# Kernel tuning notes

Hardware: AMD Instinct MI355X
Metric: run time of the kernel (lower is better)

The kernel has to match this reference:

```python
import jax, jax.numpy as jnp
import numpy as np

N_WORDS, L_CHARS = 16384, 16
CHAR_SIZE, C_EMB = 128, 64
CONV_L, KERNEL, PAD = 256, 3, 2
VOCAB, D_EMB = 50000, 300
PAD_IDX = 1


def setup_inputs() -> dict:
    key = jax.random.key(0)
    k1, k2, k3, k4, k5, k6 = jax.random.split(key, 6)
    X = jax.random.randint(k1, (N_WORDS, L_CHARS), 0, CHAR_SIZE, dtype=jnp.int32)
    X_word = jax.random.randint(k2, (N_WORDS,), 0, VOCAB, dtype=jnp.int32)
    char_emb_w = jax.random.normal(k3, (CHAR_SIZE, C_EMB), dtype=jnp.float32)
    char_emb_w = char_emb_w.at[PAD_IDX].set(0.0)  # padding row zeroed, as in _init_char_embedding
    conv_w = jax.random.normal(k4, (CONV_L, C_EMB, KERNEL), dtype=jnp.float32) * 0.05
    conv_b = jax.random.normal(k5, (CONV_L,), dtype=jnp.float32) * 0.05
    word_emb_w = jax.random.normal(k6, (VOCAB, D_EMB), dtype=jnp.float32)
    return {"X": X, "X_word": X_word, "char_emb_w": char_emb_w,
            "conv_w": conv_w, "conv_b": conv_b, "word_emb_w": word_emb_w}


def reference(X, X_word, char_emb_w, conv_w, conv_b, word_emb_w):
    # char embedding lookup: [N, L, c_emb] -> NCH layout [N, c_emb, L]
    ce = char_emb_w[X].transpose(0, 2, 1)
    # Conv1d(c_emb -> conv_l, kernel=3, padding=2): out length L + 2*PAD - K + 1
    y = jax.lax.conv_general_dilated(
        ce, conv_w, window_strides=(1,), padding=[(PAD, PAD)],
        dimension_numbers=("NCH", "OIH", "NCH"))
    y = jax.nn.relu(y + conv_b[None, :, None])
    # MaxPool over the full time dimension -> [N, conv_l]
    char_feat = jnp.max(y, axis=2)
    # word embedding lookup: [N, d_emb]
    we = word_emb_w[X_word]
    return jnp.concatenate([char_feat, we], axis=1)
```

## Files before the change

kernel.cpp:

```cpp
#include <hip/hip_runtime.h>

#define N_WORDS   16384
#define L_CHARS   16
#define CHAR_SIZE 128
#define C_EMB     64
#define CONV_L    256
#define KERNEL_K  3
#define D_EMB     300
#define OUT_STRIDE (CONV_L + D_EMB)
#define CH_Q      64
#define SLICE_H   (CHAR_SIZE * KERNEL_K * CH_Q)

typedef _Float16 half8 __attribute__((ext_vector_type(8)));

static __device__ __forceinline__ half8 h8max(half8 a, half8 b) {
#if __has_builtin(__builtin_elementwise_max)
    return __builtin_elementwise_max(a, b);
#else
    half8 r;
    #pragma unroll
    for (int i = 0; i < 8; ++i) r[i] = a[i] > b[i] ? a[i] : b[i];
    return r;
#endif
}

__global__ __launch_bounds__(384)
void build_table_fused(const float* __restrict__ emb,
                       const float* __restrict__ w,
                       _Float16* __restrict__ Th) {
    __shared__ float es[CHAR_SIZE * 65];
    __shared__ float ws[C_EMB * KERNEL_K];
    const int o = blockIdx.x;

    for (int idx = threadIdx.x; idx < CHAR_SIZE * C_EMB; idx += 384) {
        int c = idx >> 6, i = idx & 63;
        es[c * 65 + i] = emb[idx];
    }
    if (threadIdx.x < C_EMB * KERNEL_K)
        ws[threadIdx.x] = w[o * (C_EMB * KERNEL_K) + threadIdx.x];
    __syncthreads();

    const int k = threadIdx.x >> 7;
    const int c = threadIdx.x & 127;
    float s = 0.f;
    #pragma unroll
    for (int i = 0; i < C_EMB; ++i)
        s += es[c * 65 + i] * ws[i * KERNEL_K + k];

    Th[(o >> 6) * SLICE_H + c * (KERNEL_K * CH_Q) + k * CH_Q + (o & 63)]
        = (_Float16)s;
}

__global__ __launch_bounds__(256, 3)
void main_kernel(const int* __restrict__ X,
                 const int* __restrict__ Xw,
                 const _Float16* __restrict__ Th,
                 const float* __restrict__ conv_b,
                 const float* __restrict__ word_emb,
                 float* __restrict__ out,
                 int word_blocks) {
    __shared__ __align__(16) _Float16 Ts[SLICE_H];

    const int lane = threadIdx.x & 63;
    const int wv   = threadIdx.x >> 6;

    if ((int)blockIdx.x < word_blocks) {
        const int wavesTotal = word_blocks * 4;
        const int waveId = blockIdx.x * 4 + wv;
        for (int n = waveId; n < N_WORDS; n += 2 * wavesTotal) {
            const int n2 = n + wavesTotal;
            int w0 = Xw[n];
            int w1 = Xw[n2];
            const float4* s0 = (const float4*)(word_emb + (size_t)w0 * D_EMB);
            const float4* s1 = (const float4*)(word_emb + (size_t)w1 * D_EMB);
            const bool tail = lane < (D_EMB / 4 - 64);
            float4 a0 = s0[lane], a1 = s1[lane];
            float4 b0 = {}, b1 = {};
            if (tail) { b0 = s0[64 + lane]; b1 = s1[64 + lane]; }
            float4* d0 = (float4*)(out + (size_t)n  * OUT_STRIDE + CONV_L);
            float4* d1 = (float4*)(out + (size_t)n2 * OUT_STRIDE + CONV_L);
            d0[lane] = a0;
            if (tail) d0[64 + lane] = b0;
            d1[lane] = a1;
            if (tail) d1[64 + lane] = b1;
        }
        return;
    }

    const int cb   = (int)blockIdx.x - word_blocks;
    const int q    = cb & 3;
    const int wgrp = cb >> 2;

    {
        const float4* src = (const float4*)(Th + q * SLICE_H);
        float4* dst = (float4*)Ts;
        #pragma unroll
        for (int i = 0; i < 12; ++i)
            dst[threadIdx.x + i * 256] = src[threadIdx.x + i * 256];
    }
    __syncthreads();

    const int g  = lane >> 3;
    const int l8 = lane & 7;

    float bias[8];
    {
        const float4* bp = (const float4*)(conv_b + q * CH_Q + l8 * 8);
        float4 b0 = bp[0], b1 = bp[1];
        bias[0]=b0.x; bias[1]=b0.y; bias[2]=b0.z; bias[3]=b0.w;
        bias[4]=b1.x; bias[5]=b1.y; bias[6]=b1.z; bias[7]=b1.w;
    }

    int4 c0, c1, c2, c3;
    {
        const int n0 = wgrp * 128 + wv * 8 + g;
        const int4* xr = (const int4*)(X + n0 * L_CHARS);
        c0 = xr[0]; c1 = xr[1]; c2 = xr[2]; c3 = xr[3];
    }

    #pragma unroll
    for (int pass = 0; pass < 4; ++pass) {
        int4 p0 = c0, p1 = c1, p2 = c2, p3 = c3;
        if (pass < 3) {
            const int n1 = wgrp * 128 + (pass + 1) * 32 + wv * 8 + g;
            const int4* xr = (const int4*)(X + n1 * L_CHARS);
            p0 = xr[0]; p1 = xr[1]; p2 = xr[2]; p3 = xr[3];
        }

        const int n = wgrp * 128 + pass * 32 + wv * 8 + g;
        int cs[16] = {c0.x, c0.y, c0.z, c0.w,
                      c1.x, c1.y, c1.z, c1.w,
                      c2.x, c2.y, c2.z, c2.w,
                      c3.x, c3.y, c3.z, c3.w};

        half8 a0 = (half8)(_Float16)0.f;
        half8 a1 = (half8)(_Float16)0.f;
        half8 m  = (half8)(_Float16)(-65504.f);

        #pragma unroll
        for (int j = 0; j < L_CHARS; ++j) {
            const _Float16* row = Ts + cs[j] * (KERNEL_K * CH_Q) + l8 * 8;
            half8 t0 = *(const half8*)(row);
            half8 t1 = *(const half8*)(row + CH_Q);
            half8 t2 = *(const half8*)(row + 2*CH_Q);
            half8 yj = a0 + t2;
            m  = h8max(m, yj);
            a0 = a1 + t1;
            a1 = t0;
        }
        m = h8max(m, a0);
        m = h8max(m, a1);

        float r[8];
        #pragma unroll
        for (int e = 0; e < 8; ++e)
            r[e] = fmaxf((float)m[e] + bias[e], 0.f);
        float4* dst = (float4*)(out + (size_t)n * OUT_STRIDE + q * CH_Q + l8 * 8);
        dst[0] = make_float4(r[0], r[1], r[2], r[3]);
        dst[1] = make_float4(r[4], r[5], r[6], r[7]);

        c0 = p0; c1 = p1; c2 = p2; c3 = p3;
    }
}

extern "C" void kernel_launch(void* const* d_in, const int* in_sizes, int n_in,
                              void* d_out, int out_size, void* d_ws, size_t ws_size,
                              hipStream_t stream) {
    const int*   X    = (const int*)d_in[0];
    const int*   Xw   = (const int*)d_in[1];
    const float* emb  = (const float*)d_in[2];
    const float* w    = (const float*)d_in[3];
    const float* b    = (const float*)d_in[4];
    const float* we   = (const float*)d_in[5];
    float* out = (float*)d_out;

    _Float16* Th = (_Float16*)d_ws;

    build_table_fused<<<CONV_L, 384, 0, stream>>>(emb, w, Th);

    const int WB = 256;
    const int CB = 512;
    main_kernel<<<WB + CB, 256, 0, stream>>>(X, Xw, Th, b, we, out, WB);
}
```

Measured before the change: 123.5 us.

## Fuse char-conv table build into main kernel using split-fp16 MFMA

Removes the separate table-building kernel and its workspace round trip. Each conv block now computes its 128x192 slice of the char-embedding-times-conv-weight table in LDS with fp16 MFMA. Inputs are split into hi/lo halves to keep near-fp32 accuracy, and the LDS layout is XOR-swizzled to avoid bank conflicts. This saves a kernel launch and a global write/read, but every one of the 512 conv blocks recomputes the table slice it needs (each slice is rebuilt by 128 blocks), using strided uncoalesced weight loads.

```diff
diff --git a/kernel.cpp b/kernel.cpp
--- a/kernel.cpp
+++ b/kernel.cpp
@@ -10,8 +10,11 @@
 #define OUT_STRIDE (CONV_L + D_EMB)
 #define CH_Q      64
 #define SLICE_H   (CHAR_SIZE * KERNEL_K * CH_Q)
+#define WROW      (C_EMB * KERNEL_K)
 
 typedef _Float16 half8 __attribute__((ext_vector_type(8)));
+typedef _Float16 half4 __attribute__((ext_vector_type(4)));
+typedef float    f32x4 __attribute__((ext_vector_type(4)));
 
 static __device__ __forceinline__ half8 h8max(half8 a, half8 b) {
 #if __has_builtin(__builtin_elementwise_max)
@@ -24,37 +27,11 @@
 #endif
 }
 
-__global__ __launch_bounds__(384)
-void build_table_fused(const float* __restrict__ emb,
-                       const float* __restrict__ w,
-                       _Float16* __restrict__ Th) {
-    __shared__ float es[CHAR_SIZE * 65];
-    __shared__ float ws[C_EMB * KERNEL_K];
-    const int o = blockIdx.x;
-
-    for (int idx = threadIdx.x; idx < CHAR_SIZE * C_EMB; idx += 384) {
-        int c = idx >> 6, i = idx & 63;
-        es[c * 65 + i] = emb[idx];
-    }
-    if (threadIdx.x < C_EMB * KERNEL_K)
-        ws[threadIdx.x] = w[o * (C_EMB * KERNEL_K) + threadIdx.x];
-    __syncthreads();
-
-    const int k = threadIdx.x >> 7;
-    const int c = threadIdx.x & 127;
-    float s = 0.f;
-    #pragma unroll
-    for (int i = 0; i < C_EMB; ++i)
-        s += es[c * 65 + i] * ws[i * KERNEL_K + k];
-
-    Th[(o >> 6) * SLICE_H + c * (KERNEL_K * CH_Q) + k * CH_Q + (o & 63)]
-        = (_Float16)s;
-}
-
 __global__ __launch_bounds__(256, 3)
 void main_kernel(const int* __restrict__ X,
                  const int* __restrict__ Xw,
-                 const _Float16* __restrict__ Th,
+                 const float* __restrict__ emb,
+                 const float* __restrict__ w,
                  const float* __restrict__ conv_b,
                  const float* __restrict__ word_emb,
                  float* __restrict__ out,
@@ -92,11 +69,77 @@
     const int wgrp = cb >> 2;
 
     {
-        const float4* src = (const float4*)(Th + q * SLICE_H);
-        float4* dst = (float4*)Ts;
+        const int l15 = lane & 15;
+        const int lg  = lane >> 4;
+        const float* wq = w + (size_t)(q * CH_Q) * WROW;
+
         #pragma unroll
-        for (int i = 0; i < 12; ++i)
-            dst[threadIdx.x + i * 256] = src[threadIdx.x + i * 256];
+        for (int ch = 0; ch < 2; ++ch) {
+            f32x4 acc[3][4];
+            #pragma unroll
+            for (int a = 0; a < 3; ++a)
+                #pragma unroll
+                for (int b = 0; b < 4; ++b) acc[a][b] = (f32x4)0.f;
+
+            #pragma unroll
+            for (int kc = 0; kc < 2; ++kc) {
+                half8 Bh[4], Bl[4];
+                #pragma unroll
+                for (int ctl = 0; ctl < 4; ++ctl) {
+                    const int c = (ch * 4 + ctl) * 16 + l15;
+                    const float* ep = emb + c * C_EMB + kc * 32 + lg * 8;
+                    float4 v0 = *(const float4*)ep;
+                    float4 v1 = *(const float4*)(ep + 4);
+                    float vv[8] = {v0.x, v0.y, v0.z, v0.w,
+                                   v1.x, v1.y, v1.z, v1.w};
+                    #pragma unroll
+                    for (int e = 0; e < 8; ++e) {
+                        _Float16 hi = (_Float16)vv[e];
+                        Bh[ctl][e] = hi;
+                        Bl[ctl][e] = (_Float16)(vv[e] - (float)hi);
+                    }
+                }
+                #pragma unroll
+                for (int mt = 0; mt < 3; ++mt) {
+                    const int kk   = (wv * 3 + mt) * 16 + l15;
+                    const int oi   = kk & 63;
+                    const int kpos = kk >> 6;
+                    const float* ap = wq + oi * WROW + kpos
+                                      + (kc * 32 + lg * 8) * KERNEL_K;
+                    half8 Ah, Al;
+                    #pragma unroll
+                    for (int e = 0; e < 8; ++e) {
+                        float v = ap[e * KERNEL_K];
+                        _Float16 hi = (_Float16)v;
+                        Ah[e] = hi;
+                        Al[e] = (_Float16)(v - (float)hi);
+                    }
+                    #pragma unroll
+                    for (int ctl = 0; ctl < 4; ++ctl) {
+                        acc[mt][ctl] = __builtin_amdgcn_mfma_f32_16x16x32_f16(
+                            Ah, Bh[ctl], acc[mt][ctl], 0, 0, 0);
+                        acc[mt][ctl] = __builtin_amdgcn_mfma_f32_16x16x32_f16(
+                            Ah, Bl[ctl], acc[mt][ctl], 0, 0, 0);
+                        acc[mt][ctl] = __builtin_amdgcn_mfma_f32_16x16x32_f16(
+                            Al, Bh[ctl], acc[mt][ctl], 0, 0, 0);
+                    }
+                }
+            }
+            #pragma unroll
+            for (int mt = 0; mt < 3; ++mt) {
+                #pragma unroll
+                for (int ctl = 0; ctl < 4; ++ctl) {
+                    const int kk0 = (wv * 3 + mt) * 16 + lg * 4;
+                    const int c   = (ch * 4 + ctl) * 16 + l15;
+                    half4 pk;
+                    #pragma unroll
+                    for (int r = 0; r < 4; ++r)
+                        pk[r] = (_Float16)acc[mt][ctl][r];
+                    const int byte = c * 384 + ((kk0 * 2) ^ ((c & 7) << 4));
+                    *(half4*)((char*)Ts + byte) = pk;
+                }
+            }
+        }
     }
     __syncthreads();
 
@@ -139,10 +182,11 @@
 
         #pragma unroll
         for (int j = 0; j < L_CHARS; ++j) {
-            const _Float16* row = Ts + cs[j] * (KERNEL_K * CH_Q) + l8 * 8;
+            const int cc = cs[j];
+            const _Float16* row = Ts + cc * 192 + ((l8 ^ (cc & 7)) << 3);
             half8 t0 = *(const half8*)(row);
-            half8 t1 = *(const half8*)(row + CH_Q);
-            half8 t2 = *(const half8*)(row + 2*CH_Q);
+            half8 t1 = *(const half8*)(row + 64);
+            half8 t2 = *(const half8*)(row + 128);
             half8 yj = a0 + t2;
             m  = h8max(m, yj);
             a0 = a1 + t1;
@@ -173,12 +217,9 @@
     const float* b    = (const float*)d_in[4];
     const float* we   = (const float*)d_in[5];
     float* out = (float*)d_out;
-
-    _Float16* Th = (_Float16*)d_ws;
-
-    build_table_fused<<<CONV_L, 384, 0, stream>>>(emb, w, Th);
+    (void)d_ws; (void)ws_size;
 
     const int WB = 256;
     const int CB = 512;
-    main_kernel<<<WB + CB, 256, 0, stream>>>(X, Xw, Th, b, we, out, WB);
+    main_kernel<<<WB + CB, 256, 0, stream>>>(X, Xw, emb, w, b, we, out, WB);
 }
```

After: 142.1 us. +15.1%, slower.
